# Kernel optimization log

Measured on AMD Instinct MI355X. Metric: run time of the kernel, lower is better.

The kernel has to match this reference:

```python
import jax, jax.numpy as jnp
import numpy as np

N_NODES = 50000
HIDDEN = 256
ANNOT = 32
N_EDGE_TYPES = 4
EDGES_PER_TYPE = 75000
LAYER_TIMESTEPS = [3, 3]
N_LAYERS = len(LAYER_TIMESTEPS)


def setup_inputs() -> dict:
    key = jax.random.key(0)
    ks = jax.random.split(key, 12)
    x = jax.random.normal(ks[0], (N_NODES, HIDDEN), dtype=jnp.float32)
    annotations = jax.random.normal(ks[1], (N_NODES, ANNOT), dtype=jnp.float32)
    edges = jax.random.randint(ks[2], (N_EDGE_TYPES, EDGES_PER_TYPE, 2), 0, N_NODES, dtype=jnp.int64)
    s = 0.02
    # initial projection Linear(hidden+annot -> hidden)
    W_hid = jax.random.normal(ks[3], (HIDDEN, HIDDEN + ANNOT), dtype=jnp.float32) * s
    b_hid = jnp.zeros((HIDDEN,), dtype=jnp.float32)
    # per-layer, per-edge-type message linears (hidden -> hidden, with bias)
    W_msg = jax.random.normal(ks[4], (N_LAYERS, N_EDGE_TYPES, HIDDEN, HIDDEN), dtype=jnp.float32) * s
    b_msg = jnp.zeros((N_LAYERS, N_EDGE_TYPES, HIDDEN), dtype=jnp.float32)
    # per-layer GRUCell params (gate order r, z, n as in torch)
    W_ih = jax.random.normal(ks[5], (N_LAYERS, 3 * HIDDEN, HIDDEN), dtype=jnp.float32) * s
    W_hh = jax.random.normal(ks[6], (N_LAYERS, 3 * HIDDEN, HIDDEN), dtype=jnp.float32) * s
    b_ih = jnp.zeros((N_LAYERS, 3 * HIDDEN), dtype=jnp.float32)
    b_hh = jnp.zeros((N_LAYERS, 3 * HIDDEN), dtype=jnp.float32)
    return {
        'initial_node_representation': x,
        'annotations': annotations,
        'edges': edges,
        'W_hid': W_hid, 'b_hid': b_hid,
        'W_msg': W_msg, 'b_msg': b_msg,
        'W_ih': W_ih, 'W_hh': W_hh, 'b_ih': b_ih, 'b_hh': b_hh,
    }


def _gru_cell(x, h, W_ih, W_hh, b_ih, b_hh):
    # torch.nn.GRUCell math, gate order (r, z, n)
    gi = x @ W_ih.T + b_ih            # [N, 3H]
    gh = h @ W_hh.T + b_hh            # [N, 3H]
    i_r, i_z, i_n = jnp.split(gi, 3, axis=-1)
    h_r, h_z, h_n = jnp.split(gh, 3, axis=-1)
    r = jax.nn.sigmoid(i_r + h_r)
    z = jax.nn.sigmoid(i_z + h_z)
    n = jnp.tanh(i_n + r * h_n)
    return (1.0 - z) * n + z * h


def reference(initial_node_representation, annotations, edges, W_hid, b_hid,
              W_msg, b_msg, W_ih, W_hh, b_ih, b_hh):
    # initial projection of [state | annotation]
    h = jnp.concatenate([initial_node_representation, annotations], axis=1) @ W_hid.T + b_hid  # [N, H]
    n_nodes = h.shape[0]
    targets = edges[:, :, 1].reshape(-1)  # [T*E] scatter-add targets (concat over edge types)
    sources = edges[:, :, 0]              # [T, E]
    for layer in range(N_LAYERS):
        for _ in range(LAYER_TIMESTEPS[layer]):
            src_states = h[sources]  # [T, E, H] gather per edge type
            # per-edge-type linear: messages[t,e,:] = src_states[t,e,:] @ W_msg[layer,t].T + b
            msgs = jnp.einsum('teh,tgh->teg', src_states, W_msg[layer]) + b_msg[layer][:, None, :]
            msgs = msgs.reshape(-1, msgs.shape[-1])  # [T*E, H]
            incoming = jnp.zeros((n_nodes, msgs.shape[-1]), dtype=h.dtype).at[targets].add(msgs)
            h = _gru_cell(incoming, h, W_ih[layer], W_hh[layer], b_ih[layer], b_hh[layer])
    return h  # nodelevel=True -> last layer node states [N, H]
```

## Files before the change

### kernel.cpp

```cpp
#include <hip/hip_runtime.h>

#define N_NODES 50000
#define HIDDEN  256
#define ANNOT   32
#define NTYPES  4
#define EPT     75000
#define CAPA    32

typedef __attribute__((ext_vector_type(4))) float    f32x4;
typedef __attribute__((ext_vector_type(8))) _Float16 f16x8;
typedef __attribute__((ext_vector_type(4))) _Float16 f16x4;
typedef _Float16 half_t;

#define MFMA16(a,b,c) __builtin_amdgcn_mfma_f32_16x16x32_f16((a),(b),(c),0,0,0)

__device__ __forceinline__ void gload16(const void* g, void* l) {
    __builtin_amdgcn_global_load_lds((const __attribute__((address_space(1))) void*)g,
                                     (__attribute__((address_space(3))) void*)l, 16, 0, 0);
}

__global__ void k_cvt(const float* __restrict__ in, half_t* __restrict__ out, int n) {
    int i = blockIdx.x * blockDim.x + threadIdx.x;
    if (i < n) out[i] = (half_t)in[i];
}

__global__ void k_cvt_wg(const float* __restrict__ Wih, const float* __restrict__ Whh,
                         half_t* __restrict__ out) {
    int i = blockIdx.x * blockDim.x + threadIdx.x;
    if (i >= 786432) return;
    const int e = i & 7; int idx = i >> 3;
    const int gcol = idx % 384; idx /= 384;
    const int kc = idx & 3; idx >>= 2;
    const int chunk = idx & 15; idx >>= 4;
    const int yb = idx & 1;
    const int layer = idx >> 1;
    const int gate = gcol >> 7, cl = gcol & 127;
    const int k = chunk * 32 + kc * 8 + e;
    const int colf = gate * 256 + yb * 128 + cl;
    float v = (k < 256) ? Whh[((size_t)layer * 768 + colf) * 256 + k]
                        : Wih[((size_t)layer * 768 + colf) * 256 + (k - 256)];
    out[i] = (half_t)v;
}

__global__ void k_cvt_wy(const float* __restrict__ Wmsg, half_t* __restrict__ out) {
    int i = blockIdx.x * blockDim.x + threadIdx.x;
    if (i >= 524288) return;
    const int e = i & 7; int idx = i >> 3;
    const int col = idx & 255; idx >>= 8;
    const int kc = idx & 3; idx >>= 2;
    const int chunk = idx & 7; idx >>= 3;
    const int yb = idx & 3;
    const int layer = idx >> 2;
    const int k = chunk * 32 + kc * 8 + e;
    out[i] = (half_t)Wmsg[(((size_t)layer * 4 + yb) * 256 + col) * 256 + k];
}

__global__ void k_csr2(const int* __restrict__ edges, int* __restrict__ cnt_all,
                       int* __restrict__ cnt4, int* __restrict__ elist) {
    int i = blockIdx.x * blockDim.x + threadIdx.x;
    if (i >= NTYPES * EPT) return;
    int2 st = *reinterpret_cast<const int2*>(&edges[(size_t)i * 2]);
    const int tt = i / EPT;
    atomicAdd(&cnt4[tt * N_NODES + st.y], 1);
    int pos = atomicAdd(&cnt_all[st.y], 1);
    if (pos < CAPA) elist[(size_t)st.y * CAPA + pos] = st.x * 4 + tt;
}

__global__ __launch_bounds__(256) void k_init(
    const float* __restrict__ x, const float* __restrict__ annot,
    const half_t* __restrict__ Whid16, const float* __restrict__ b_hid,
    half_t* __restrict__ h16out)
{
    __shared__ __align__(16) half_t Atile[4 * 64 * 8];
    const int tid  = threadIdx.x;
    const int lane = tid & 63;
    const int wave = tid >> 6;
    const int n0   = blockIdx.x * 64;

    f32x4 acc[4][4] = {};

    for (int ks = 0; ks < 9; ++ks) {
        const int k0 = ks * 32;
        {
            const int c = tid >> 6, r = tid & 63;
            const int node = n0 + r;
            f16x8 hv = {};
            if (node < N_NODES) {
                const int kk = k0 + c * 8;
                const float* s = (kk < HIDDEN) ? (x + (size_t)node * HIDDEN + kk)
                                               : (annot + (size_t)node * ANNOT + (kk - HIDDEN));
                const float4* s4 = reinterpret_cast<const float4*>(s);
                float4 a0 = s4[0], a1 = s4[1];
                hv[0]=(half_t)a0.x; hv[1]=(half_t)a0.y; hv[2]=(half_t)a0.z; hv[3]=(half_t)a0.w;
                hv[4]=(half_t)a1.x; hv[5]=(half_t)a1.y; hv[6]=(half_t)a1.z; hv[7]=(half_t)a1.w;
            }
            *reinterpret_cast<f16x8*>(&Atile[(c * 64 + r) * 8]) = hv;
        }
        __syncthreads();
        const int kc = lane >> 4, rl = lane & 15;
        f16x8 af[4];
        #pragma unroll
        for (int rt = 0; rt < 4; ++rt)
            af[rt] = *reinterpret_cast<const f16x8*>(&Atile[(kc * 64 + rt * 16 + rl) * 8]);
        #pragma unroll
        for (int nt = 0; nt < 4; ++nt) {
            const int col = wave * 64 + nt * 16 + rl;
            f16x8 bf = *reinterpret_cast<const f16x8*>(&Whid16[col * 288 + k0 + kc * 8]);
            #pragma unroll
            for (int rt = 0; rt < 4; ++rt)
                acc[rt][nt] = MFMA16(af[rt], bf, acc[rt][nt]);
        }
        __syncthreads();
    }

    const int rl = lane & 15, rg = lane >> 4;
    #pragma unroll
    for (int rt = 0; rt < 4; ++rt)
        #pragma unroll
        for (int i = 0; i < 4; ++i) {
            const int row = n0 + rt * 16 + rg * 4 + i;
            if (row >= N_NODES) continue;
            #pragma unroll
            for (int nt = 0; nt < 4; ++nt) {
                const int col = wave * 64 + nt * 16 + rl;
                h16out[(size_t)row * 256 + col] = (half_t)(acc[rt][nt][i] + b_hid[col]);
            }
        }
}

__global__ __launch_bounds__(512, 2) void k_y4(
    const half_t* __restrict__ h16in, const half_t* __restrict__ Wy,
    half_t* __restrict__ Y, int layer)
{
    __shared__ __align__(16) half_t lds[20480];
    const int t = threadIdx.x, lane = t & 63;
    const int rh = (t >> 6) >> 2, wc = (t >> 6) & 3;
    const int n0 = blockIdx.x * 64;
    const int kc = lane >> 4, rl = lane & 15;

    int nodeA = n0 + (t >> 2); if (nodeA > N_NODES - 1) nodeA = N_NODES - 1;
    const half_t* aA = h16in + (size_t)nodeA * 256 + (t & 3) * 8;
    const half_t* pB = Wy + (size_t)layer * 262144 + (size_t)t * 8;

    #pragma unroll 1
    for (int yb = 0; yb < 4; ++yb) {
        f32x4 acc[2][4] = {};
        {
            const half_t* s0 = pB + (size_t)(yb * 8) * 8192;
            gload16(s0,        lds + t * 8);
            gload16(s0 + 4096, lds + 4096 + t * 8);
            if (t < 256) gload16(aA, lds + 8192 + t * 8);
        }
        __syncthreads();
        #pragma unroll 1
        for (int c = 0; c < 8; ++c) {
            const int cur = c & 1;
            half_t* bB = lds + (cur ? 10240 : 0);
            if (c < 7) {
                half_t* nB = lds + (cur ? 0 : 10240);
                const half_t* sn = pB + (size_t)(yb * 8 + c + 1) * 8192;
                gload16(sn,        nB + t * 8);
                gload16(sn + 4096, nB + 4096 + t * 8);
                if (t < 256) gload16(aA + (c + 1) * 32, nB + 8192 + t * 8);
            }
            f16x8 af[2];
            #pragma unroll
            for (int rt = 0; rt < 2; ++rt)
                af[rt] = *reinterpret_cast<const f16x8*>(
                    &bB[8192 + ((rh * 32 + rt * 16 + rl) * 4 + kc) * 8]);
            const half_t* Bq = bB + (size_t)(kc * 256 + wc * 64 + rl) * 8;
            #pragma unroll
            for (int nt = 0; nt < 4; ++nt) {
                f16x8 bf = *reinterpret_cast<const f16x8*>(Bq + nt * 128);
                #pragma unroll
                for (int rt = 0; rt < 2; ++rt)
                    acc[rt][nt] = MFMA16(af[rt], bf, acc[rt][nt]);
            }
            __syncthreads();
        }
        const int rg = kc;
        #pragma unroll
        for (int rt = 0; rt < 2; ++rt)
            #pragma unroll
            for (int i = 0; i < 4; ++i) {
                const int row = rh * 32 + rt * 16 + rg * 4 + i;
                #pragma unroll
                for (int nt = 0; nt < 4; ++nt)
                    lds[row * 264 + wc * 64 + nt * 16 + rl] = (half_t)acc[rt][nt][i];
            }
        __syncthreads();
        #pragma unroll
        for (int p = 0; p < 4; ++p) {
            const int g = p * 512 + t, row = g >> 5, q = g & 31;
            if (n0 + row < N_NODES)
                *reinterpret_cast<f16x8*>(&Y[(size_t)(n0 + row) * 1024 + yb * 256 + q * 8]) =
                    *reinterpret_cast<const f16x8*>(&lds[row * 264 + q * 8]);
        }
        __syncthreads();
    }
}

__global__ __launch_bounds__(256) void k_gather2(
    const half_t* __restrict__ Y, const int* __restrict__ cnt_all,
    const int* __restrict__ cnt4, const int* __restrict__ elist,
    const float* __restrict__ b_msg, half_t* __restrict__ inc16, int layer)
{
    const int wave = threadIdx.x >> 6, lane = threadIdx.x & 63;
    const int v = blockIdx.x * 4 + wave;
    if (v >= N_NODES) return;
    int c = cnt_all[v]; if (c > CAPA) c = CAPA;
    const int* el = elist + (size_t)v * CAPA;
    float s0 = 0.f, s1 = 0.f, s2 = 0.f, s3 = 0.f;
    for (int e = 0; e < c; ++e) {
        const int packed = el[e];
        f16x4 y = *reinterpret_cast<const f16x4*>(&Y[(size_t)packed * 256 + lane * 4]);
        s0 += (float)y[0]; s1 += (float)y[1]; s2 += (float)y[2]; s3 += (float)y[3];
    }
    const float4* bm = reinterpret_cast<const float4*>(b_msg + (size_t)layer * 1024);
    #pragma unroll
    for (int tt = 0; tt < 4; ++tt) {
        const float fc = (float)cnt4[tt * N_NODES + v];
        float4 b = bm[tt * 64 + lane];
        s0 += fc * b.x; s1 += fc * b.y; s2 += fc * b.z; s3 += fc * b.w;
    }
    f16x4 o; o[0] = (half_t)s0; o[1] = (half_t)s1; o[2] = (half_t)s2; o[3] = (half_t)s3;
    *reinterpret_cast<f16x4*>(&inc16[(size_t)v * 256 + lane * 4]) = o;
}

#define GRU_COMPUTE(BB, AN) do {                                                        \
    f16x8 af[2];                                                                        \
    _Pragma("unroll")                                                                   \
    for (int rt = 0; rt < 2; ++rt)                                                      \
        af[rt] = *reinterpret_cast<const f16x8*>(                                       \
            &(BB)[12288 + ((rh * 32 + rt * 16 + rl) * 4 + kc) * 8]);                    \
    const half_t* Bq_ = (BB) + (size_t)(kc * 384 + wc * 32 + rl) * 8;                   \
    _Pragma("unroll")                                                                   \
    for (int nt = 0; nt < 2; ++nt) {                                                    \
        f16x8 br_ = *reinterpret_cast<const f16x8*>(Bq_ + nt * 128);                    \
        f16x8 bz_ = *reinterpret_cast<const f16x8*>(Bq_ + 1024 + nt * 128);             \
        f16x8 bn_ = *reinterpret_cast<const f16x8*>(Bq_ + 2048 + nt * 128);             \
        _Pragma("unroll")                                                               \
        for (int rt = 0; rt < 2; ++rt) {                                                \
            ar[rt][nt] = MFMA16(af[rt], br_, ar[rt][nt]);                               \
            az[rt][nt] = MFMA16(af[rt], bz_, az[rt][nt]);                               \
            AN[rt][nt] = MFMA16(af[rt], bn_, AN[rt][nt]);                               \
        }                                                                               \
    }                                                                                   \
} while (0)

#define GRU_STAGE(cc, DST, ASRC) do {                                                   \
    const half_t* sn_ = pB + (size_t)(yb * 16 + (cc)) * 12288;                          \
    gload16(sn_,        (DST) + t * 8);                                                 \
    gload16(sn_ + 4096, (DST) + 4096 + t * 8);                                          \
    gload16(sn_ + 8192, (DST) + 8192 + t * 8);                                          \
    if (t < 256) gload16((ASRC), (DST) + 12288 + t * 8);                                \
} while (0)

__global__ __launch_bounds__(512, 2) void k_gru5(
    const half_t* __restrict__ h16in, const half_t* __restrict__ inc16,
    half_t* __restrict__ h16out, float* __restrict__ out32,
    const half_t* __restrict__ Wg,
    const float* __restrict__ b_ih, const float* __restrict__ b_hh,
    int layer, int last)
{
    __shared__ __align__(16) half_t lds[28672];
    const int t = threadIdx.x, lane = t & 63;
    const int rh = (t >> 6) >> 2, wc = (t >> 6) & 3;
    const int n0 = blockIdx.x * 64;
    const int kc = lane >> 4, rl = lane & 15;

    int nodeA = n0 + (t >> 2); if (nodeA > N_NODES - 1) nodeA = N_NODES - 1;
    const half_t* aH = h16in + (size_t)nodeA * 256 + (t & 3) * 8;
    const half_t* aI = inc16 + (size_t)nodeA * 256 + (t & 3) * 8;
    const half_t* pB = Wg + (size_t)layer * 393216 + (size_t)t * 8;

    const float* bi = b_ih + layer * 768;
    const float* bh = b_hh + layer * 768;

    #pragma unroll 1
    for (int yb = 0; yb < 2; ++yb) {
        f32x4 ar[2][2] = {}, az[2][2] = {}, ahn[2][2] = {}, ain[2][2] = {};

        GRU_STAGE(0, lds, aH);
        __syncthreads();

        #pragma unroll 1
        for (int c = 0; c < 8; ++c) {
            const int cur = c & 1;
            half_t* bB = lds + (cur ? 14336 : 0);
            half_t* nB = lds + (cur ? 0 : 14336);
            const half_t* sa = (c < 7) ? (aH + (c + 1) * 32) : aI;
            GRU_STAGE(c + 1, nB, sa);
            GRU_COMPUTE(bB, ahn);
            __syncthreads();
        }
        #pragma unroll 1
        for (int c = 8; c < 16; ++c) {
            const int cur = c & 1;
            half_t* bB = lds + (cur ? 14336 : 0);
            if (c < 15) {
                half_t* nB = lds + (cur ? 0 : 14336);
                GRU_STAGE(c + 1, nB, aI + (c - 7) * 32);
            }
            GRU_COMPUTE(bB, ain);
            __syncthreads();
        }

        const int rg = kc;
        #pragma unroll
        for (int rt = 0; rt < 2; ++rt)
            #pragma unroll
            for (int i = 0; i < 4; ++i) {
                const int row = n0 + rh * 32 + rt * 16 + rg * 4 + i;
                const bool ok = row < N_NODES;
                #pragma unroll
                for (int nt = 0; nt < 2; ++nt) {
                    const int col = yb * 128 + wc * 32 + nt * 16 + rl;
                    float sr  = ar [rt][nt][i] + bi[col]       + bh[col];
                    float sz  = az [rt][nt][i] + bi[256 + col] + bh[256 + col];
                    float xin = ain[rt][nt][i] + bi[512 + col];
                    float xhn = ahn[rt][nt][i] + bh[512 + col];
                    float r = 1.f / (1.f + __expf(-sr));
                    float z = 1.f / (1.f + __expf(-sz));
                    float a = xin + r * xhn;
                    float e2 = __expf(2.f * a);
                    float n = (e2 - 1.f) / (e2 + 1.f);
                    float hold = ok ? (float)h16in[(size_t)row * 256 + col] : 0.f;
                    ar[rt][nt][i] = (1.f - z) * n + z * hold;
                }
            }

        if (!last) {
            #pragma unroll
            for (int rt = 0; rt < 2; ++rt)
                #pragma unroll
                for (int i = 0; i < 4; ++i) {
                    const int rr = rh * 32 + rt * 16 + rg * 4 + i;
                    #pragma unroll
                    for (int nt = 0; nt < 2; ++nt)
                        lds[rr * 136 + wc * 32 + nt * 16 + rl] = (half_t)ar[rt][nt][i];
                }
            __syncthreads();
            #pragma unroll
            for (int p = 0; p < 2; ++p) {
                const int g = p * 512 + t, row = g >> 4, q = g & 15;
                if (n0 + row < N_NODES)
                    *reinterpret_cast<f16x8*>(&h16out[(size_t)(n0 + row) * 256 + yb * 128 + q * 8]) =
                        *reinterpret_cast<const f16x8*>(&lds[row * 136 + q * 8]);
            }
            __syncthreads();
        } else {
            #pragma unroll
            for (int rt = 0; rt < 2; ++rt)
                #pragma unroll
                for (int i = 0; i < 4; ++i) {
                    const int row = n0 + rh * 32 + rt * 16 + rg * 4 + i;
                    if (row >= N_NODES) continue;
                    #pragma unroll
                    for (int nt = 0; nt < 2; ++nt) {
                        const int col = yb * 128 + wc * 32 + nt * 16 + rl;
                        out32[(size_t)row * 256 + col] = ar[rt][nt][i];
                    }
                }
        }
    }
}

extern "C" void kernel_launch(void* const* d_in, const int* in_sizes, int n_in,
                              void* d_out, int out_size, void* d_ws, size_t ws_size,
                              hipStream_t stream) {
    const float* x      = (const float*)d_in[0];
    const float* annot  = (const float*)d_in[1];
    const int*   edges  = (const int*)  d_in[2];
    const float* W_hid  = (const float*)d_in[3];
    const float* b_hid  = (const float*)d_in[4];
    const float* W_msg  = (const float*)d_in[5];
    const float* b_msg  = (const float*)d_in[6];
    const float* W_ih   = (const float*)d_in[7];
    const float* W_hh   = (const float*)d_in[8];
    const float* b_ih   = (const float*)d_in[9];
    const float* b_hh   = (const float*)d_in[10];

    char* ws = (char*)d_ws;
    size_t off = 0;
    auto alloc = [&](size_t bytes) -> char* {
        char* p = ws + off;
        off = (off + bytes + 255) & ~(size_t)255;
        return p;
    };
    half_t* hA      = (half_t*)alloc((size_t)N_NODES * 256 * 2);
    half_t* hB      = (half_t*)alloc((size_t)N_NODES * 256 * 2);
    half_t* inc16   = (half_t*)alloc((size_t)N_NODES * 256 * 2);
    half_t* Y       = (half_t*)alloc((size_t)N_NODES * 1024 * 2);
    int*    elist   = (int*)   alloc((size_t)N_NODES * CAPA * 4);
    int*    cnt_all = (int*)   alloc((size_t)N_NODES * 4);
    int*    cnt4    = (int*)   alloc((size_t)NTYPES * N_NODES * 4);
    half_t* Whid16  = (half_t*)alloc((size_t)256 * 288 * 2);
    half_t* Wg      = (half_t*)alloc((size_t)786432 * 2);
    half_t* Wy      = (half_t*)alloc((size_t)524288 * 2);
    (void)ws_size;

    hipMemsetAsync(cnt_all, 0, (size_t)N_NODES * 4, stream);
    hipMemsetAsync(cnt4,    0, (size_t)NTYPES * N_NODES * 4, stream);
    k_csr2<<<dim3((NTYPES * EPT + 255) / 256), 256, 0, stream>>>(edges, cnt_all, cnt4, elist);
    k_cvt<<<dim3((73728 + 255) / 256), 256, 0, stream>>>(W_hid, Whid16, 73728);
    k_cvt_wg<<<dim3(786432 / 256), 256, 0, stream>>>(W_ih, W_hh, Wg);
    k_cvt_wy<<<dim3(524288 / 256), 256, 0, stream>>>(W_msg, Wy);

    const int NB = (N_NODES + 63) / 64;
    k_init<<<dim3(NB), 256, 0, stream>>>(x, annot, Whid16, b_hid, hA);

    for (int step = 0; step < 6; ++step) {
        const int layer = step / 3;
        half_t* hin  = (step & 1) ? hB : hA;
        half_t* hout = (step & 1) ? hA : hB;
        const int last = (step == 5) ? 1 : 0;
        k_y4<<<dim3(NB), 512, 0, stream>>>(hin, Wy, Y, layer);
        k_gather2<<<dim3((N_NODES + 3) / 4), 256, 0, stream>>>(
            Y, cnt_all, cnt4, elist, b_msg, inc16, layer);
        k_gru5<<<dim3(NB), 512, 0, stream>>>(
            hin, inc16, hout, (float*)d_out, Wg, b_ih, b_hh, layer, last);
    }
}
```

Measured before the change: 1.419 ms.

## Split output column blocks across grid y and load A fragments directly from global

The per-block serial loop over output column blocks in the message GEMM and GRU GEMM kernels becomes a second grid dimension, giving 4x and 2x more blocks. Activation fragments are now read straight from global memory into registers and double-buffered, rather than staged through LDS. LDS use shrinks and launch bounds rise, aiming for higher occupancy and more parallelism. The cost is that each block re-reads the node rows it needs, adding global traffic for the activations.

```diff
diff --git a/kernel.cpp b/kernel.cpp
--- a/kernel.cpp
+++ b/kernel.cpp
@@ -128,75 +128,84 @@
         }
 }
 
-__global__ __launch_bounds__(512, 2) void k_y4(
+#define Y5_STAGE(cc, DST) do {                                                         \
+    const half_t* sn_ = pBy + (size_t)(cc) * 8192;                                     \
+    gload16(sn_ + t * 8,        (DST) + t * 8);                                        \
+    gload16(sn_ + 4096 + t * 8, (DST) + 4096 + t * 8);                                 \
+} while (0)
+
+#define Y5_LOADA(AF, cc) do {                                                          \
+    _Pragma("unroll") for (int rt = 0; rt < 2; ++rt)                                   \
+        (AF)[rt] = *reinterpret_cast<const f16x8*>(apY[rt] + (cc) * 32);               \
+} while (0)
+
+#define Y5_COMP(AF, BUF) do {                                                          \
+    const half_t* Bq_ = (BUF) + (size_t)(kc * 256 + wc * 64 + rl) * 8;                 \
+    _Pragma("unroll") for (int nt = 0; nt < 4; ++nt) {                                 \
+        f16x8 bf_ = *reinterpret_cast<const f16x8*>(Bq_ + nt * 128);                   \
+        _Pragma("unroll") for (int rt = 0; rt < 2; ++rt)                               \
+            acc[rt][nt] = MFMA16((AF)[rt], bf_, acc[rt][nt]);                          \
+    }                                                                                  \
+} while (0)
+
+__global__ __launch_bounds__(512, 8) void k_y5(
     const half_t* __restrict__ h16in, const half_t* __restrict__ Wy,
     half_t* __restrict__ Y, int layer)
 {
-    __shared__ __align__(16) half_t lds[20480];
+    __shared__ __align__(16) half_t lds[16896];
     const int t = threadIdx.x, lane = t & 63;
     const int rh = (t >> 6) >> 2, wc = (t >> 6) & 3;
-    const int n0 = blockIdx.x * 64;
+    const int n0 = blockIdx.x * 64, yb = blockIdx.y;
     const int kc = lane >> 4, rl = lane & 15;
 
-    int nodeA = n0 + (t >> 2); if (nodeA > N_NODES - 1) nodeA = N_NODES - 1;
-    const half_t* aA = h16in + (size_t)nodeA * 256 + (t & 3) * 8;
-    const half_t* pB = Wy + (size_t)layer * 262144 + (size_t)t * 8;
+    const half_t* apY[2];
+    #pragma unroll
+    for (int rt = 0; rt < 2; ++rt) {
+        int node = n0 + rh * 32 + rt * 16 + rl;
+        if (node > N_NODES - 1) node = N_NODES - 1;
+        apY[rt] = h16in + (size_t)node * 256 + kc * 8;
+    }
+    const half_t* pBy = Wy + (size_t)(layer * 4 + yb) * 65536;
+    half_t* buf0 = lds; half_t* buf1 = lds + 8192;
+
+    f32x4 acc[2][4] = {};
+    f16x8 afA[2], afB[2];
+
+    Y5_STAGE(0, buf0);
+    Y5_LOADA(afA, 0);
+    __syncthreads();
 
     #pragma unroll 1
-    for (int yb = 0; yb < 4; ++yb) {
-        f32x4 acc[2][4] = {};
-        {
-            const half_t* s0 = pB + (size_t)(yb * 8) * 8192;
-            gload16(s0,        lds + t * 8);
-            gload16(s0 + 4096, lds + 4096 + t * 8);
-            if (t < 256) gload16(aA, lds + 8192 + t * 8);
-        }
-        __syncthreads();
-        #pragma unroll 1
-        for (int c = 0; c < 8; ++c) {
-            const int cur = c & 1;
-            half_t* bB = lds + (cur ? 10240 : 0);
-            if (c < 7) {
-                half_t* nB = lds + (cur ? 0 : 10240);
-                const half_t* sn = pB + (size_t)(yb * 8 + c + 1) * 8192;
-                gload16(sn,        nB + t * 8);
-                gload16(sn + 4096, nB + 4096 + t * 8);
-                if (t < 256) gload16(aA + (c + 1) * 32, nB + 8192 + t * 8);
-            }
-            f16x8 af[2];
-            #pragma unroll
-            for (int rt = 0; rt < 2; ++rt)
-                af[rt] = *reinterpret_cast<const f16x8*>(
-                    &bB[8192 + ((rh * 32 + rt * 16 + rl) * 4 + kc) * 8]);
-            const half_t* Bq = bB + (size_t)(kc * 256 + wc * 64 + rl) * 8;
-            #pragma unroll
-            for (int nt = 0; nt < 4; ++nt) {
-                f16x8 bf = *reinterpret_cast<const f16x8*>(Bq + nt * 128);
-                #pragma unroll
-                for (int rt = 0; rt < 2; ++rt)
-                    acc[rt][nt] = MFMA16(af[rt], bf, acc[rt][nt]);
-            }
-            __syncthreads();
-        }
-        const int rg = kc;
-        #pragma unroll
-        for (int rt = 0; rt < 2; ++rt)
-            #pragma unroll
-            for (int i = 0; i < 4; ++i) {
-                const int row = rh * 32 + rt * 16 + rg * 4 + i;
-                #pragma unroll
-                for (int nt = 0; nt < 4; ++nt)
-                    lds[row * 264 + wc * 64 + nt * 16 + rl] = (half_t)acc[rt][nt][i];
-            }
-        __syncthreads();
-        #pragma unroll
-        for (int p = 0; p < 4; ++p) {
-            const int g = p * 512 + t, row = g >> 5, q = g & 31;
-            if (n0 + row < N_NODES)
-                *reinterpret_cast<f16x8*>(&Y[(size_t)(n0 + row) * 1024 + yb * 256 + q * 8]) =
-                    *reinterpret_cast<const f16x8*>(&lds[row * 264 + q * 8]);
-        }
-        __syncthreads();
+    for (int p = 0; p < 4; ++p) {
+        Y5_STAGE(2 * p + 1, buf1);
+        Y5_LOADA(afB, 2 * p + 1);
+        Y5_COMP(afA, buf0);
+        __syncthreads();
+        if (p < 3) {
+            Y5_STAGE(2 * p + 2, buf0);
+            Y5_LOADA(afA, 2 * p + 2);
+        }
+        Y5_COMP(afB, buf1);
+        __syncthreads();
+    }
+
+    const int rg = kc;
+    #pragma unroll
+    for (int rt = 0; rt < 2; ++rt)
+        #pragma unroll
+        for (int i = 0; i < 4; ++i) {
+            const int row = rh * 32 + rt * 16 + rg * 4 + i;
+            #pragma unroll
+            for (int nt = 0; nt < 4; ++nt)
+                lds[row * 264 + wc * 64 + nt * 16 + rl] = (half_t)acc[rt][nt][i];
+        }
+    __syncthreads();
+    #pragma unroll
+    for (int p = 0; p < 4; ++p) {
+        const int g = p * 512 + t, row = g >> 5, q = g & 31;
+        if (n0 + row < N_NODES)
+            *reinterpret_cast<f16x8*>(&Y[(size_t)(n0 + row) * 1024 + yb * 256 + q * 8]) =
+                *reinterpret_cast<const f16x8*>(&lds[row * 264 + q * 8]);
     }
 }
 
@@ -227,142 +236,148 @@
     *reinterpret_cast<f16x4*>(&inc16[(size_t)v * 256 + lane * 4]) = o;
 }
 
-#define GRU_COMPUTE(BB, AN) do {                                                        \
-    f16x8 af[2];                                                                        \
-    _Pragma("unroll")                                                                   \
-    for (int rt = 0; rt < 2; ++rt)                                                      \
-        af[rt] = *reinterpret_cast<const f16x8*>(                                       \
-            &(BB)[12288 + ((rh * 32 + rt * 16 + rl) * 4 + kc) * 8]);                    \
-    const half_t* Bq_ = (BB) + (size_t)(kc * 384 + wc * 32 + rl) * 8;                   \
-    _Pragma("unroll")                                                                   \
-    for (int nt = 0; nt < 2; ++nt) {                                                    \
-        f16x8 br_ = *reinterpret_cast<const f16x8*>(Bq_ + nt * 128);                    \
-        f16x8 bz_ = *reinterpret_cast<const f16x8*>(Bq_ + 1024 + nt * 128);             \
-        f16x8 bn_ = *reinterpret_cast<const f16x8*>(Bq_ + 2048 + nt * 128);             \
-        _Pragma("unroll")                                                               \
-        for (int rt = 0; rt < 2; ++rt) {                                                \
-            ar[rt][nt] = MFMA16(af[rt], br_, ar[rt][nt]);                               \
-            az[rt][nt] = MFMA16(af[rt], bz_, az[rt][nt]);                               \
-            AN[rt][nt] = MFMA16(af[rt], bn_, AN[rt][nt]);                               \
-        }                                                                               \
-    }                                                                                   \
-} while (0)
-
-#define GRU_STAGE(cc, DST, ASRC) do {                                                   \
-    const half_t* sn_ = pB + (size_t)(yb * 16 + (cc)) * 12288;                          \
-    gload16(sn_,        (DST) + t * 8);                                                 \
-    gload16(sn_ + 4096, (DST) + 4096 + t * 8);                                          \
-    gload16(sn_ + 8192, (DST) + 8192 + t * 8);                                          \
-    if (t < 256) gload16((ASRC), (DST) + 12288 + t * 8);                                \
-} while (0)
-
-__global__ __launch_bounds__(512, 2) void k_gru5(
+#define GRU6_STAGE(cc, DST) do {                                                       \
+    const half_t* sn_ = pB + (size_t)(cc) * 12288;                                     \
+    gload16(sn_ + t * 8,        (DST) + t * 8);                                        \
+    gload16(sn_ + 4096 + t * 8, (DST) + 4096 + t * 8);                                 \
+    gload16(sn_ + 8192 + t * 8, (DST) + 8192 + t * 8);                                 \
+} while (0)
+
+#define GRU6_LOADA(AF, cc) do {                                                        \
+    const int c_ = (cc);                                                               \
+    _Pragma("unroll") for (int rt = 0; rt < 2; ++rt)                                   \
+        (AF)[rt] = *reinterpret_cast<const f16x8*>(                                    \
+            (c_ < 8 ? apH[rt] : apI[rt]) + (c_ & 7) * 32);                             \
+} while (0)
+
+#define GRU6_COMP(AF, BUF, AN) do {                                                    \
+    const half_t* Bq_ = (BUF) + (size_t)(kc * 384 + wc * 32 + rl) * 8;                 \
+    _Pragma("unroll") for (int nt = 0; nt < 2; ++nt) {                                 \
+        f16x8 br_ = *reinterpret_cast<const f16x8*>(Bq_ + nt * 128);                   \
+        f16x8 bz_ = *reinterpret_cast<const f16x8*>(Bq_ + 1024 + nt * 128);            \
+        f16x8 bn_ = *reinterpret_cast<const f16x8*>(Bq_ + 2048 + nt * 128);            \
+        _Pragma("unroll") for (int rt = 0; rt < 2; ++rt) {                             \
+            ar[rt][nt] = MFMA16((AF)[rt], br_, ar[rt][nt]);                            \
+            az[rt][nt] = MFMA16((AF)[rt], bz_, az[rt][nt]);                            \
+            AN[rt][nt] = MFMA16((AF)[rt], bn_, AN[rt][nt]);                            \
+        }                                                                              \
+    }                                                                                  \
+} while (0)
+
+__global__ __launch_bounds__(512, 6) void k_gru6(
     const half_t* __restrict__ h16in, const half_t* __restrict__ inc16,
     half_t* __restrict__ h16out, float* __restrict__ out32,
     const half_t* __restrict__ Wg,
     const float* __restrict__ b_ih, const float* __restrict__ b_hh,
     int layer, int last)
 {
-    __shared__ __align__(16) half_t lds[28672];
+    __shared__ __align__(16) half_t lds[24576];
     const int t = threadIdx.x, lane = t & 63;
     const int rh = (t >> 6) >> 2, wc = (t >> 6) & 3;
-    const int n0 = blockIdx.x * 64;
+    const int n0 = blockIdx.x * 64, yb = blockIdx.y;
     const int kc = lane >> 4, rl = lane & 15;
 
-    int nodeA = n0 + (t >> 2); if (nodeA > N_NODES - 1) nodeA = N_NODES - 1;
-    const half_t* aH = h16in + (size_t)nodeA * 256 + (t & 3) * 8;
-    const half_t* aI = inc16 + (size_t)nodeA * 256 + (t & 3) * 8;
-    const half_t* pB = Wg + (size_t)layer * 393216 + (size_t)t * 8;
-
+    const half_t* apH[2];
+    const half_t* apI[2];
+    #pragma unroll
+    for (int rt = 0; rt < 2; ++rt) {
+        int node = n0 + rh * 32 + rt * 16 + rl;
+        if (node > N_NODES - 1) node = N_NODES - 1;
+        apH[rt] = h16in + (size_t)node * 256 + kc * 8;
+        apI[rt] = inc16 + (size_t)node * 256 + kc * 8;
+    }
+    const half_t* pB = Wg + (size_t)(layer * 2 + yb) * 196608;
+    half_t* buf0 = lds; half_t* buf1 = lds + 12288;
+
+    f32x4 ar[2][2] = {}, az[2][2] = {}, ahn[2][2] = {}, ain[2][2] = {};
+    f16x8 afA[2], afB[2];
+
+    GRU6_STAGE(0, buf0);
+    GRU6_LOADA(afA, 0);
+    __syncthreads();
+
+    #pragma unroll 1
+    for (int p = 0; p < 4; ++p) {
+        GRU6_STAGE(2 * p + 1, buf1);
+        GRU6_LOADA(afB, 2 * p + 1);
+        GRU6_COMP(afA, buf0, ahn);
+        __syncthreads();
+        GRU6_STAGE(2 * p + 2, buf0);
+        GRU6_LOADA(afA, 2 * p + 2);
+        GRU6_COMP(afB, buf1, ahn);
+        __syncthreads();
+    }
+    #pragma unroll 1
+    for (int p = 4; p < 8; ++p) {
+        GRU6_STAGE(2 * p + 1, buf1);
+        GRU6_LOADA(afB, 2 * p + 1);
+        GRU6_COMP(afA, buf0, ain);
+        __syncthreads();
+        if (p < 7) {
+            GRU6_STAGE(2 * p + 2, buf0);
+            GRU6_LOADA(afA, 2 * p + 2);
+        }
+        GRU6_COMP(afB, buf1, ain);
+        __syncthreads();
+    }
+
+    const int rg = kc;
     const float* bi = b_ih + layer * 768;
     const float* bh = b_hh + layer * 768;
-
-    #pragma unroll 1
-    for (int yb = 0; yb < 2; ++yb) {
-        f32x4 ar[2][2] = {}, az[2][2] = {}, ahn[2][2] = {}, ain[2][2] = {};
-
-        GRU_STAGE(0, lds, aH);
-        __syncthreads();
-
-        #pragma unroll 1
-        for (int c = 0; c < 8; ++c) {
-            const int cur = c & 1;
-            half_t* bB = lds + (cur ? 14336 : 0);
-            half_t* nB = lds + (cur ? 0 : 14336);
-            const half_t* sa = (c < 7) ? (aH + (c + 1) * 32) : aI;
-            GRU_STAGE(c + 1, nB, sa);
-            GRU_COMPUTE(bB, ahn);
-            __syncthreads();
-        }
-        #pragma unroll 1
-        for (int c = 8; c < 16; ++c) {
-            const int cur = c & 1;
-            half_t* bB = lds + (cur ? 14336 : 0);
-            if (c < 15) {
-                half_t* nB = lds + (cur ? 0 : 14336);
-                GRU_STAGE(c + 1, nB, aI + (c - 7) * 32);
+    #pragma unroll
+    for (int rt = 0; rt < 2; ++rt)
+        #pragma unroll
+        for (int i = 0; i < 4; ++i) {
+            const int row = n0 + rh * 32 + rt * 16 + rg * 4 + i;
+            const bool ok = row < N_NODES;
+            #pragma unroll
+            for (int nt = 0; nt < 2; ++nt) {
+                const int col = yb * 128 + wc * 32 + nt * 16 + rl;
+                float sr  = ar [rt][nt][i] + bi[col]       + bh[col];
+                float sz  = az [rt][nt][i] + bi[256 + col] + bh[256 + col];
+                float xin = ain[rt][nt][i] + bi[512 + col];
+                float xhn = ahn[rt][nt][i] + bh[512 + col];
+                float r = 1.f / (1.f + __expf(-sr));
+                float z = 1.f / (1.f + __expf(-sz));
+                float a = xin + r * xhn;
+                float e2 = __expf(2.f * a);
+                float n = (e2 - 1.f) / (e2 + 1.f);
+                float hold = ok ? (float)h16in[(size_t)row * 256 + col] : 0.f;
+                ar[rt][nt][i] = (1.f - z) * n + z * hold;
             }
-            GRU_COMPUTE(bB, ain);
-            __syncthreads();
-        }
-
-        const int rg = kc;
+        }
+
+    if (!last) {
+        #pragma unroll
+        for (int rt = 0; rt < 2; ++rt)
+            #pragma unroll
+            for (int i = 0; i < 4; ++i) {
+                const int rr = rh * 32 + rt * 16 + rg * 4 + i;
+                #pragma unroll
+                for (int nt = 0; nt < 2; ++nt)
+                    lds[rr * 136 + wc * 32 + nt * 16 + rl] = (half_t)ar[rt][nt][i];
+            }
+        __syncthreads();
+        #pragma unroll
+        for (int p = 0; p < 2; ++p) {
+            const int g = p * 512 + t, row = g >> 4, q = g & 15;
+            if (n0 + row < N_NODES)
+                *reinterpret_cast<f16x8*>(&h16out[(size_t)(n0 + row) * 256 + yb * 128 + q * 8]) =
+                    *reinterpret_cast<const f16x8*>(&lds[row * 136 + q * 8]);
+        }
+    } else {
         #pragma unroll
         for (int rt = 0; rt < 2; ++rt)
             #pragma unroll
             for (int i = 0; i < 4; ++i) {
                 const int row = n0 + rh * 32 + rt * 16 + rg * 4 + i;
-                const bool ok = row < N_NODES;
+                if (row >= N_NODES) continue;
                 #pragma unroll
                 for (int nt = 0; nt < 2; ++nt) {
                     const int col = yb * 128 + wc * 32 + nt * 16 + rl;
-                    float sr  = ar [rt][nt][i] + bi[col]       + bh[col];
-                    float sz  = az [rt][nt][i] + bi[256 + col] + bh[256 + col];
-                    float xin = ain[rt][nt][i] + bi[512 + col];
-                    float xhn = ahn[rt][nt][i] + bh[512 + col];
-                    float r = 1.f / (1.f + __expf(-sr));
-                    float z = 1.f / (1.f + __expf(-sz));
-                    float a = xin + r * xhn;
-                    float e2 = __expf(2.f * a);
-                    float n = (e2 - 1.f) / (e2 + 1.f);
-                    float hold = ok ? (float)h16in[(size_t)row * 256 + col] : 0.f;
-                    ar[rt][nt][i] = (1.f - z) * n + z * hold;
+                    out32[(size_t)row * 256 + col] = ar[rt][nt][i];
                 }
             }
-
-        if (!last) {
-            #pragma unroll
-            for (int rt = 0; rt < 2; ++rt)
-                #pragma unroll
-                for (int i = 0; i < 4; ++i) {
-                    const int rr = rh * 32 + rt * 16 + rg * 4 + i;
-                    #pragma unroll
-                    for (int nt = 0; nt < 2; ++nt)
-                        lds[rr * 136 + wc * 32 + nt * 16 + rl] = (half_t)ar[rt][nt][i];
-                }
-            __syncthreads();
-            #pragma unroll
-            for (int p = 0; p < 2; ++p) {
-                const int g = p * 512 + t, row = g >> 4, q = g & 15;
-                if (n0 + row < N_NODES)
-                    *reinterpret_cast<f16x8*>(&h16out[(size_t)(n0 + row) * 256 + yb * 128 + q * 8]) =
-                        *reinterpret_cast<const f16x8*>(&lds[row * 136 + q * 8]);
-            }
-            __syncthreads();
-        } else {
-            #pragma unroll
-            for (int rt = 0; rt < 2; ++rt)
-                #pragma unroll
-                for (int i = 0; i < 4; ++i) {
-                    const int row = n0 + rh * 32 + rt * 16 + rg * 4 + i;
-                    if (row >= N_NODES) continue;
-                    #pragma unroll
-                    for (int nt = 0; nt < 2; ++nt) {
-                        const int col = yb * 128 + wc * 32 + nt * 16 + rl;
-                        out32[(size_t)row * 256 + col] = ar[rt][nt][i];
-                    }
-                }
-        }
     }
 }
 
@@ -415,10 +430,10 @@
         half_t* hin  = (step & 1) ? hB : hA;
         half_t* hout = (step & 1) ? hA : hB;
         const int last = (step == 5) ? 1 : 0;
-        k_y4<<<dim3(NB), 512, 0, stream>>>(hin, Wy, Y, layer);
+        k_y5<<<dim3(NB, 4), 512, 0, stream>>>(hin, Wy, Y, layer);
         k_gather2<<<dim3((N_NODES + 3) / 4), 256, 0, stream>>>(
             Y, cnt_all, cnt4, elist, b_msg, inc16, layer);
-        k_gru5<<<dim3(NB), 512, 0, stream>>>(
+        k_gru6<<<dim3(NB, 2), 512, 0, stream>>>(
             hin, inc16, hout, (float*)d_out, Wg, b_ih, b_hh, layer, last);
     }
 }
```

Result: slower. 1.964 ms (+38.4%).
